# Performance work log

Measured on AMD Instinct MI355X. Metric: run time of the kernel, lower is better.

## Reference

```python
import jax, jax.numpy as jnp
import numpy as np

L = 3          # num_modification_layers
MOD_SCALE = 0.01


def setup_inputs() -> dict:
    key = jax.random.key(0)
    B, E = 8192, 1024
    ks = jax.random.split(key, 12)
    sg = 1.0 / np.sqrt(E)        # GRUCell / Linear(E,.) init bound
    sh = 1.0 / np.sqrt(E // 2)   # Linear(E//2, E) init bound
    u = lambda k, shape, s: jax.random.uniform(k, shape, jnp.float32, -s, s)
    return {
        "x":    jax.random.normal(ks[0], (B, E), jnp.float32),
        # GRUCell params (PyTorch layout: gates ordered r, z, n)
        "W_ih": u(ks[1], (L, 3 * E, E), sg),
        "W_hh": u(ks[2], (L, 3 * E, E), sg),
        "b_ih": u(ks[3], (L, 3 * E), sg),
        "b_hh": u(ks[4], (L, 3 * E), sg),
        # modification network: Linear(E, E//2) -> ReLU -> Linear(E//2, E) -> Tanh
        "W1":   u(ks[5], (L, E // 2, E), sg),
        "b1":   u(ks[6], (L, E // 2), sg),
        "W2":   u(ks[7], (L, E, E // 2), sh),
        "b2":   u(ks[8], (L, E), sh),
        # modification gate: Linear(E, 1) -> Sigmoid
        "Wg":   u(ks[9], (L, 1, E), sg),
        "bg":   u(ks[10], (L, 1), sg),
    }


def reference(x, W_ih, W_hh, b_ih, b_hh, W1, b1, W2, b2, Wg, bg):
    B, E = x.shape
    h_prev = jnp.zeros((B, E), x.dtype)  # hidden states reset to zeros
    cur = x
    for l in range(L):
        # modification network (small MLP) + scalar gate
        sig = jnp.tanh(jax.nn.relu(cur @ W1[l].T + b1[l]) @ W2[l].T + b2[l])  # (B, E)
        gate = jax.nn.sigmoid(cur @ Wg[l].T + bg[l])                           # (B, 1)
        cond = jnp.mean(gate) > 0.5
        # data-dependent self-modification: weight_ih += scale * mean(sig)[None,:]
        # (row-broadcast over the 3E gate rows), predicated on-device
        wih = jnp.where(cond,
                        W_ih[l] + MOD_SCALE * jnp.mean(sig, axis=0)[None, :],
                        W_ih[l])
        # GRUCell (PyTorch semantics)
        gi = cur @ wih.T + b_ih[l]            # (B, 3E)
        gh = h_prev @ W_hh[l].T + b_hh[l]     # (B, 3E) -- h_prev is zeros
        i_r, i_z, i_n = jnp.split(gi, 3, axis=1)
        h_r, h_z, h_n = jnp.split(gh, 3, axis=1)
        r = jax.nn.sigmoid(i_r + h_r)
        z = jax.nn.sigmoid(i_z + h_z)
        n = jnp.tanh(i_n + r * h_n)
        h = (1.0 - z) * n + z * h_prev
        cur = h + sig
    return cur
```

## Files before the change

kernel.cpp:

```cpp
#include <hip/hip_runtime.h>
#include <cstdint>
#include <cstddef>


#define BSZ 8192
#define ESZ 1024

typedef _Float16 f16x8 __attribute__((ext_vector_type(8)));
typedef float    f32x4 __attribute__((ext_vector_type(4)));
typedef unsigned short u16;
typedef u16 u16x4 __attribute__((ext_vector_type(4)));

__device__ __forceinline__ u16 f2h(float f) {
    _Float16 h = (_Float16)f;
    return __builtin_bit_cast(u16, h);
}
__device__ __forceinline__ float h2f(u16 h) {
    return (float)__builtin_bit_cast(_Float16, h);
}

__device__ __forceinline__ void gload16(const void* g, void* l) {
    __builtin_amdgcn_global_load_lds((const __attribute__((address_space(1))) void*)g,
                                     (__attribute__((address_space(3))) void*)l,
                                     16, 0, 0);
}

__device__ __forceinline__ int swzi(int row, int chunk) {
    return (row << 6) + (((chunk ^ row) & 7) << 3);
}

__device__ __forceinline__ float sigmoidf_(float x) {
    return 1.f / (1.f + __expf(-x));
}
__device__ __forceinline__ float tanhf_(float x) {
    float cx = fminf(fmaxf(x, -15.f), 15.f);
    float e = __expf(2.f * cx);
    return (e - 1.f) / (e + 1.f);
}

#define N4_WIH (3 * 3072 * 1024 / 4)
#define N4_W1  (3 * 512 * 1024 / 4)
#define N4_W2  (3 * 1024 * 512 / 4)
#define N4_X   (BSZ * ESZ / 4)

__global__ void cvt_all_kernel(const float* __restrict__ Wih, const float* __restrict__ W1,
                               const float* __restrict__ W2, const float* __restrict__ x,
                               u16* __restrict__ oWih, u16* __restrict__ oW1,
                               u16* __restrict__ oW2, u16* __restrict__ ox) {
    int i = blockIdx.x * 256 + threadIdx.x;
    const float* in;
    u16* out;
    if (i < N4_WIH) { in = Wih; out = oWih; }
    else if (i < N4_WIH + N4_W1) { i -= N4_WIH; in = W1; out = oW1; }
    else if (i < N4_WIH + N4_W1 + N4_W2) { i -= N4_WIH + N4_W1; in = W2; out = oW2; }
    else { i -= N4_WIH + N4_W1 + N4_W2; if (i >= N4_X) return; in = x; out = ox; }
    f32x4 v = ((const f32x4*)in)[i];
    u16x4 o;
    o.x = f2h(v.x); o.y = f2h(v.y); o.z = f2h(v.z); o.w = f2h(v.w);
    ((u16x4*)out)[i] = o;
}

__global__ void gate_kernel(const u16* __restrict__ cur, const float* __restrict__ Wg,
                            const float* __restrict__ bg, const float* __restrict__ colsum,
                            float* __restrict__ gsum, float* __restrict__ sdot) {
    const int wid = threadIdx.x >> 6, lane = threadIdx.x & 63;
    const int row = blockIdx.x * 4 + wid;
    const u16* cr = cur + (size_t)row * ESZ;
    float pg = 0.f, pm = 0.f;
#pragma unroll
    for (int h = 0; h < 2; h++) {
        int base = lane * 16 + h * 8;
        f16x8 cv = *(const f16x8*)(cr + base);
#pragma unroll
        for (int q = 0; q < 2; q++) {
            f32x4 wv = *(const f32x4*)(Wg + base + q * 4);
            f32x4 mv = *(const f32x4*)(colsum + base + q * 4);
#pragma unroll
            for (int e = 0; e < 4; e++) {
                float c = (float)cv[q * 4 + e];
                pg += c * wv[e];
                pm += c * mv[e];
            }
        }
    }
#pragma unroll
    for (int s = 32; s >= 1; s >>= 1) {
        pg += __shfl_xor(pg, s);
        pm += __shfl_xor(pm, s);
    }
    __shared__ float gp[4];
    if (lane == 0) {
        gp[wid] = sigmoidf_(pg + bg[0]);
        sdot[row] = pm * (0.01f / 8192.f);
    }
    __syncthreads();
    if (threadIdx.x == 0) atomicAdd(gsum, gp[0] + gp[1] + gp[2] + gp[3]);
}

template <int ACT>
__global__ void __launch_bounds__(256, 2) gemm_act_kernel(
    const u16* __restrict__ A, const u16* __restrict__ W,
    const float* __restrict__ bias, u16* __restrict__ outp,
    float* __restrict__ colsum, int N, int K) {
    __shared__ u16 lA[128 * 64];
    __shared__ u16 lB[128 * 64];
    const int t = threadIdx.x;
    const int m0 = blockIdx.y * 128, n0 = blockIdx.x * 128;
    const int wid = t >> 6, lane = t & 63;
    const int waver = wid >> 1, wavec = wid & 1;
    const int lrow = lane & 15, lk = lane >> 4;

    f32x4 acc[4][4] = {};

    for (int k0 = 0; k0 < K; k0 += 64) {
        __syncthreads();
#pragma unroll
        for (int i = 0; i < 4; i++) {
            int eo = i * 2048 + t * 8;
            int r = eo >> 6;
            int gc = (((eo >> 3) ^ r) & 7) << 3;
            gload16(A + (size_t)(m0 + r) * K + k0 + gc, &lA[eo]);
            gload16(W + (size_t)(n0 + r) * K + k0 + gc, &lB[eo]);
        }
        __syncthreads();
#pragma unroll
        for (int kk = 0; kk < 2; kk++) {
            f16x8 af[4], bf[4];
#pragma unroll
            for (int m = 0; m < 4; m++)
                af[m] = *(const f16x8*)&lA[swzi(waver * 64 + m * 16 + lrow, kk * 4 + lk)];
#pragma unroll
            for (int n = 0; n < 4; n++)
                bf[n] = *(const f16x8*)&lB[swzi(wavec * 64 + n * 16 + lrow, kk * 4 + lk)];
#pragma unroll
            for (int m = 0; m < 4; m++)
#pragma unroll
                for (int n = 0; n < 4; n++)
                    acc[m][n] = __builtin_amdgcn_mfma_f32_16x16x32_f16(af[m], bf[n], acc[m][n], 0, 0, 0);
        }
    }

#pragma unroll
    for (int n = 0; n < 4; n++) {
        int c = n0 + wavec * 64 + n * 16 + lrow;
        float bv = bias[c];
        float cs = 0.f;
#pragma unroll
        for (int m = 0; m < 4; m++) {
            int rbase = m0 + waver * 64 + m * 16 + lk * 4;
#pragma unroll
            for (int j = 0; j < 4; j++) {
                float v = acc[m][n][j] + bv;
                if (ACT == 0) {
                    v = v > 0.f ? v : 0.f;
                    outp[(size_t)(rbase + j) * N + c] = f2h(v);
                } else {
                    float tv = tanhf_(v);
                    outp[(size_t)(rbase + j) * N + c] = f2h(tv);
                    cs += tv;
                }
            }
        }
        if (ACT == 1) {
            cs += __shfl_xor(cs, 16);
            cs += __shfl_xor(cs, 32);
            if (lane < 16) atomicAdd(&colsum[c], cs);
        }
    }
}

__global__ void __launch_bounds__(256, 2) gemm_gru_kernel(
    const u16* __restrict__ Ab, const u16* __restrict__ Wb,
    const float* __restrict__ bih, const float* __restrict__ bhh,
    const u16* __restrict__ sig, const float* __restrict__ sdot,
    const float* __restrict__ gsum, float* __restrict__ curf_out,
    u16* __restrict__ curb_out) {
    __shared__ u16 lA[2][128 * 64];
    __shared__ u16 lB[2][3][64 * 64];
    const int t = threadIdx.x;
    const int hw = blockIdx.y * 16 + blockIdx.x;
    const int xcd = hw & 7, idx = hw >> 3;
    const int m0 = (idx >> 1) * 128, c0 = ((xcd << 1) | (idx & 1)) * 64;
    const int wid = t >> 6, lane = t & 63;
    const int waver = wid >> 1, wavec = wid & 1;
    const int lrow = lane & 15, lk = lane >> 4;
    const int K = ESZ, E = ESZ;

    const int eoA = t * 8;
    f32x4 acc[4][6] = {};

    auto STAGE = [&](int buf, int k0) {
#pragma unroll
        for (int i = 0; i < 4; i++) {
            int eo = i * 2048 + eoA;
            int r = eo >> 6;
            int gc = (((eo >> 3) ^ r) & 7) << 3;
            gload16(Ab + (size_t)(m0 + r) * K + k0 + gc, &lA[buf][eo]);
        }
#pragma unroll
        for (int g = 0; g < 3; g++)
#pragma unroll
            for (int i = 0; i < 2; i++) {
                int eo = i * 2048 + eoA;
                int r = eo >> 6;
                int gc = (((eo >> 3) ^ r) & 7) << 3;
                gload16(Wb + (size_t)(g * 1024 + c0 + r) * K + k0 + gc, &lB[buf][g][eo]);
            }
    };

    STAGE(0, 0);
    int cur = 0;
    for (int kt = 0; kt < 16; ++kt) {
        __syncthreads();
        if (kt < 15) STAGE(cur ^ 1, (kt + 1) * 64);
#pragma unroll
        for (int kk = 0; kk < 2; kk++) {
            f16x8 af[4];
#pragma unroll
            for (int m = 0; m < 4; m++)
                af[m] = *(const f16x8*)&lA[cur][swzi(waver * 64 + m * 16 + lrow, kk * 4 + lk)];
#pragma unroll
            for (int g = 0; g < 3; g++) {
#pragma unroll
                for (int n = 0; n < 2; n++) {
                    f16x8 bf = *(const f16x8*)&lB[cur][g][swzi(wavec * 32 + n * 16 + lrow, kk * 4 + lk)];
#pragma unroll
                    for (int m = 0; m < 4; m++)
                        acc[m][g * 2 + n] =
                            __builtin_amdgcn_mfma_f32_16x16x32_f16(af[m], bf, acc[m][g * 2 + n], 0, 0, 0);
                }
            }
        }
        cur ^= 1;
    }

    const bool cond = (*gsum) > 4096.f;
#pragma unroll
    for (int m = 0; m < 4; m++) {
        int rbase = m0 + waver * 64 + m * 16 + lk * 4;
        float corr[4];
#pragma unroll
        for (int j = 0; j < 4; j++) corr[j] = cond ? sdot[rbase + j] : 0.f;
#pragma unroll
        for (int n = 0; n < 2; n++) {
            int c = c0 + wavec * 32 + n * 16 + lrow;
            float br = bih[c], bz = bih[E + c], bn = bih[2 * E + c];
            float hr = bhh[c], hz = bhh[E + c], hn = bhh[2 * E + c];
#pragma unroll
            for (int j = 0; j < 4; j++) {
                float ir = acc[m][0 + n][j] + br + corr[j];
                float iz = acc[m][2 + n][j] + bz + corr[j];
                float inn = acc[m][4 + n][j] + bn + corr[j];
                float r = sigmoidf_(ir + hr);
                float z = sigmoidf_(iz + hz);
                float nn = tanhf_(inn + r * hn);
                float h = (1.f - z) * nn;
                float o = h + h2f(sig[(size_t)(rbase + j) * E + c]);
                if (curf_out) curf_out[(size_t)(rbase + j) * E + c] = o;
                if (curb_out) curb_out[(size_t)(rbase + j) * E + c] = f2h(o);
            }
        }
    }
}

extern "C" void kernel_launch(void* const* d_in, const int* in_sizes, int n_in,
                              void* d_out, int out_size, void* d_ws, size_t ws_size,
                              hipStream_t stream) {
    const float* x   = (const float*)d_in[0];
    const float* Wih = (const float*)d_in[1];
    const float* bih = (const float*)d_in[3];
    const float* bhh = (const float*)d_in[4];
    const float* W1  = (const float*)d_in[5];
    const float* b1  = (const float*)d_in[6];
    const float* W2  = (const float*)d_in[7];
    const float* b2  = (const float*)d_in[8];
    const float* Wg  = (const float*)d_in[9];
    const float* bg  = (const float*)d_in[10];
    float* out = (float*)d_out;

    char* w = (char*)d_ws;
    u16* Wihb  = (u16*)w;  w += (size_t)3 * 3072 * 1024 * 2;
    u16* W1b   = (u16*)w;  w += (size_t)3 * 512 * 1024 * 2;
    u16* W2b   = (u16*)w;  w += (size_t)3 * 1024 * 512 * 2;
    u16* curbA = (u16*)w;  w += (size_t)BSZ * ESZ * 2;
    u16* curbB = (u16*)w;  w += (size_t)BSZ * ESZ * 2;
    u16* Amat  = (u16*)w;  w += (size_t)BSZ * 512 * 2;
    u16* sigb  = (u16*)w;  w += (size_t)BSZ * ESZ * 2;
    float* colsum = (float*)w;  w += 4096;
    float* gsum   = (float*)w;  w += 256;
    float* sdot   = (float*)w;  w += (size_t)BSZ * 4;

    {
        int n4 = N4_WIH + N4_W1 + N4_W2 + N4_X;
        cvt_all_kernel<<<dim3((n4 + 255) / 256), 256, 0, stream>>>(
            Wih, W1, W2, x, Wihb, W1b, W2b, curbA);
    }

    u16* cin = curbA;
    u16* cout = curbB;
    for (int l = 0; l < 3; l++) {
        hipMemsetAsync(colsum, 0, 4096 + 4, stream);
        gemm_act_kernel<0><<<dim3(512 / 128, BSZ / 128), 256, 0, stream>>>(
            cin, W1b + (size_t)l * 512 * 1024, b1 + l * 512, Amat, nullptr, 512, 1024);
        gemm_act_kernel<1><<<dim3(1024 / 128, BSZ / 128), 256, 0, stream>>>(
            Amat, W2b + (size_t)l * 1024 * 512, b2 + l * 1024, sigb, colsum, 1024, 512);
        gate_kernel<<<dim3(BSZ / 4), 256, 0, stream>>>(
            cin, Wg + l * 1024, bg + l, colsum, gsum, sdot);
        gemm_gru_kernel<<<dim3(16, BSZ / 128), 256, 0, stream>>>(
            cin, Wihb + (size_t)l * 3072 * 1024, bih + l * 3072, bhh + l * 3072,
            sigb, sdot, gsum, (l == 2) ? out : nullptr, (l < 2) ? cout : nullptr);
        u16* tmp = cin; cin = cout; cout = tmp;
    }
}
```

Before: 595.5 us.

## Use 128x64 tiles, double-buffered LDS, and XCD-aware block remap in MLP GEMMs

The two modification-MLP GEMM kernels move from 128x128 to 128x64 output tiles, which doubles the grid size (256→512 and 512→1024 blocks) and raises the occupancy hint to 3 blocks per CU. Global-to-LDS loads are now double-buffered so the next K-slice is fetched while the current one feeds the MFMAs. Block IDs are remapped across the 8 XCDs so that neighbouring tiles land on the same XCD, which should improve L2 reuse. The cost is less reuse of A per tile, more total A traffic, and a larger LDS footprint per block.

After: 582.3 us. 2.2% less time.

```diff
diff --git a/kernel.cpp b/kernel.cpp
--- a/kernel.cpp
+++ b/kernel.cpp
@@ -98,51 +98,68 @@
 }
 
 template <int ACT>
-__global__ void __launch_bounds__(256, 2) gemm_act_kernel(
+__global__ void __launch_bounds__(256, 3) gemm_act_kernel(
     const u16* __restrict__ A, const u16* __restrict__ W,
     const float* __restrict__ bias, u16* __restrict__ outp,
-    float* __restrict__ colsum, int N, int K) {
-    __shared__ u16 lA[128 * 64];
-    __shared__ u16 lB[128 * 64];
+    float* __restrict__ colsum, int N, int K, int nshift) {
+    __shared__ u16 lA[2][128 * 64];
+    __shared__ u16 lB[2][64 * 64];
     const int t = threadIdx.x;
-    const int m0 = blockIdx.y * 128, n0 = blockIdx.x * 128;
+    const int chunk = gridDim.x >> 3;
+    const int o = blockIdx.x;
+    const int tl = (o & 7) * chunk + (o >> 3);
+    const int m0 = (tl >> nshift) * 128;
+    const int n0 = (tl & ((1 << nshift) - 1)) * 64;
     const int wid = t >> 6, lane = t & 63;
     const int waver = wid >> 1, wavec = wid & 1;
     const int lrow = lane & 15, lk = lane >> 4;
 
-    f32x4 acc[4][4] = {};
-
-    for (int k0 = 0; k0 < K; k0 += 64) {
-        __syncthreads();
+    f32x4 acc[4][2] = {};
+
+    auto STAGE = [&](int buf, int k0) {
 #pragma unroll
         for (int i = 0; i < 4; i++) {
             int eo = i * 2048 + t * 8;
             int r = eo >> 6;
             int gc = (((eo >> 3) ^ r) & 7) << 3;
-            gload16(A + (size_t)(m0 + r) * K + k0 + gc, &lA[eo]);
-            gload16(W + (size_t)(n0 + r) * K + k0 + gc, &lB[eo]);
-        }
+            gload16(A + (size_t)(m0 + r) * K + k0 + gc, &lA[buf][eo]);
+        }
+#pragma unroll
+        for (int i = 0; i < 2; i++) {
+            int eo = i * 2048 + t * 8;
+            int r = eo >> 6;
+            int gc = (((eo >> 3) ^ r) & 7) << 3;
+            gload16(W + (size_t)(n0 + r) * K + k0 + gc, &lB[buf][eo]);
+        }
+    };
+
+    STAGE(0, 0);
+    const int nk = K >> 6;
+    int cur = 0;
+    for (int kt = 0; kt < nk; ++kt) {
         __syncthreads();
+        if (kt + 1 < nk) STAGE(cur ^ 1, (kt + 1) * 64);
 #pragma unroll
         for (int kk = 0; kk < 2; kk++) {
-            f16x8 af[4], bf[4];
+            f16x8 af[4], bf[2];
 #pragma unroll
             for (int m = 0; m < 4; m++)
-                af[m] = *(const f16x8*)&lA[swzi(waver * 64 + m * 16 + lrow, kk * 4 + lk)];
-#pragma unroll
-            for (int n = 0; n < 4; n++)
-                bf[n] = *(const f16x8*)&lB[swzi(wavec * 64 + n * 16 + lrow, kk * 4 + lk)];
+                af[m] = *(const f16x8*)&lA[cur][swzi(waver * 64 + m * 16 + lrow, kk * 4 + lk)];
+#pragma unroll
+            for (int n = 0; n < 2; n++)
+                bf[n] = *(const f16x8*)&lB[cur][swzi(wavec * 32 + n * 16 + lrow, kk * 4 + lk)];
 #pragma unroll
             for (int m = 0; m < 4; m++)
 #pragma unroll
-                for (int n = 0; n < 4; n++)
+                for (int n = 0; n < 2; n++)
                     acc[m][n] = __builtin_amdgcn_mfma_f32_16x16x32_f16(af[m], bf[n], acc[m][n], 0, 0, 0);
         }
-    }
-
-#pragma unroll
-    for (int n = 0; n < 4; n++) {
-        int c = n0 + wavec * 64 + n * 16 + lrow;
+        cur ^= 1;
+    }
+
+#pragma unroll
+    for (int n = 0; n < 2; n++) {
+        int c = n0 + wavec * 32 + n * 16 + lrow;
         float bv = bias[c];
         float cs = 0.f;
 #pragma unroll
@@ -300,10 +317,10 @@
     u16* cout = curbB;
     for (int l = 0; l < 3; l++) {
         hipMemsetAsync(colsum, 0, 4096 + 4, stream);
-        gemm_act_kernel<0><<<dim3(512 / 128, BSZ / 128), 256, 0, stream>>>(
-            cin, W1b + (size_t)l * 512 * 1024, b1 + l * 512, Amat, nullptr, 512, 1024);
-        gemm_act_kernel<1><<<dim3(1024 / 128, BSZ / 128), 256, 0, stream>>>(
-            Amat, W2b + (size_t)l * 1024 * 512, b2 + l * 1024, sigb, colsum, 1024, 512);
+        gemm_act_kernel<0><<<dim3(512), 256, 0, stream>>>(
+            cin, W1b + (size_t)l * 512 * 1024, b1 + l * 512, Amat, nullptr, 512, 1024, 3);
+        gemm_act_kernel<1><<<dim3(1024), 256, 0, stream>>>(
+            Amat, W2b + (size_t)l * 1024 * 512, b2 + l * 1024, sigb, colsum, 1024, 512, 4);
         gate_kernel<<<dim3(BSZ / 4), 256, 0, stream>>>(
             cin, Wg + l * 1024, bg + l, colsum, gsum, sdot);
         gemm_gru_kernel<<<dim3(16, BSZ / 128), 256, 0, stream>>>(
```

## Unify GEMMs into one 512-thread double-buffered kernel with 256-row tiles

Applied to the files above, without the earlier changes.

Replaces the separate activation GEMM and GRU GEMM kernels with a single templated kernel. It uses 512 threads (8 waves), 256-row A tiles, double-buffered LDS staging and XCD-aware block mapping. The MLP GEMMs now get the prefetch pipelining the GRU GEMM already had, and larger M tiles reuse each staged B tile across more rows. The cost is more LDS per block (the GRU variant needs about 128KB with double buffering), which can lower occupancy. Narrower 64-column N tiles for the MLP GEMMs mean the A tile is reloaded more often.

After: 581.0 us. -2.4%, faster.

```diff
diff --git a/kernel.cpp b/kernel.cpp
--- a/kernel.cpp
+++ b/kernel.cpp
@@ -97,122 +97,50 @@
     if (threadIdx.x == 0) atomicAdd(gsum, gp[0] + gp[1] + gp[2] + gp[3]);
 }
 
-template <int ACT>
-__global__ void __launch_bounds__(256, 2) gemm_act_kernel(
+template <int NG, int EPI>
+__global__ void __launch_bounds__(512, 2) gemm_fused_kernel(
     const u16* __restrict__ A, const u16* __restrict__ W,
-    const float* __restrict__ bias, u16* __restrict__ outp,
-    float* __restrict__ colsum, int N, int K) {
-    __shared__ u16 lA[128 * 64];
-    __shared__ u16 lB[128 * 64];
+    const float* __restrict__ bias, const float* __restrict__ bhh,
+    const u16* __restrict__ sig, const float* __restrict__ sdot,
+    const float* __restrict__ gsum, u16* __restrict__ outp,
+    float* __restrict__ curf_out, float* __restrict__ colsum,
+    int K, int NC) {
+    __shared__ u16 lA[2][256 * 64];
+    __shared__ u16 lB[2][NG][64 * 64];
     const int t = threadIdx.x;
-    const int m0 = blockIdx.y * 128, n0 = blockIdx.x * 128;
+    const int xcd = blockIdx.x & 7, q = blockIdx.x >> 3;
+    const int m0 = (xcd * 4 + (q & 3)) * 256;
+    const int c0 = (q >> 2) * 64;
     const int wid = t >> 6, lane = t & 63;
     const int waver = wid >> 1, wavec = wid & 1;
     const int lrow = lane & 15, lk = lane >> 4;
-
-    f32x4 acc[4][4] = {};
-
-    for (int k0 = 0; k0 < K; k0 += 64) {
-        __syncthreads();
+    const int E = ESZ;
+
+    f32x4 acc[4][2 * NG] = {};
+
+    auto STAGE = [&](int buf, int k0) {
 #pragma unroll
         for (int i = 0; i < 4; i++) {
-            int eo = i * 2048 + t * 8;
+            int eo = i * 4096 + t * 8;
             int r = eo >> 6;
             int gc = (((eo >> 3) ^ r) & 7) << 3;
-            gload16(A + (size_t)(m0 + r) * K + k0 + gc, &lA[eo]);
-            gload16(W + (size_t)(n0 + r) * K + k0 + gc, &lB[eo]);
-        }
-        __syncthreads();
-#pragma unroll
-        for (int kk = 0; kk < 2; kk++) {
-            f16x8 af[4], bf[4];
-#pragma unroll
-            for (int m = 0; m < 4; m++)
-                af[m] = *(const f16x8*)&lA[swzi(waver * 64 + m * 16 + lrow, kk * 4 + lk)];
-#pragma unroll
-            for (int n = 0; n < 4; n++)
-                bf[n] = *(const f16x8*)&lB[swzi(wavec * 64 + n * 16 + lrow, kk * 4 + lk)];
-#pragma unroll
-            for (int m = 0; m < 4; m++)
-#pragma unroll
-                for (int n = 0; n < 4; n++)
-                    acc[m][n] = __builtin_amdgcn_mfma_f32_16x16x32_f16(af[m], bf[n], acc[m][n], 0, 0, 0);
-        }
-    }
-
-#pragma unroll
-    for (int n = 0; n < 4; n++) {
-        int c = n0 + wavec * 64 + n * 16 + lrow;
-        float bv = bias[c];
-        float cs = 0.f;
-#pragma unroll
-        for (int m = 0; m < 4; m++) {
-            int rbase = m0 + waver * 64 + m * 16 + lk * 4;
-#pragma unroll
-            for (int j = 0; j < 4; j++) {
-                float v = acc[m][n][j] + bv;
-                if (ACT == 0) {
-                    v = v > 0.f ? v : 0.f;
-                    outp[(size_t)(rbase + j) * N + c] = f2h(v);
-                } else {
-                    float tv = tanhf_(v);
-                    outp[(size_t)(rbase + j) * N + c] = f2h(tv);
-                    cs += tv;
-                }
-            }
-        }
-        if (ACT == 1) {
-            cs += __shfl_xor(cs, 16);
-            cs += __shfl_xor(cs, 32);
-            if (lane < 16) atomicAdd(&colsum[c], cs);
-        }
-    }
-}
-
-__global__ void __launch_bounds__(256, 2) gemm_gru_kernel(
-    const u16* __restrict__ Ab, const u16* __restrict__ Wb,
-    const float* __restrict__ bih, const float* __restrict__ bhh,
-    const u16* __restrict__ sig, const float* __restrict__ sdot,
-    const float* __restrict__ gsum, float* __restrict__ curf_out,
-    u16* __restrict__ curb_out) {
-    __shared__ u16 lA[2][128 * 64];
-    __shared__ u16 lB[2][3][64 * 64];
-    const int t = threadIdx.x;
-    const int hw = blockIdx.y * 16 + blockIdx.x;
-    const int xcd = hw & 7, idx = hw >> 3;
-    const int m0 = (idx >> 1) * 128, c0 = ((xcd << 1) | (idx & 1)) * 64;
-    const int wid = t >> 6, lane = t & 63;
-    const int waver = wid >> 1, wavec = wid & 1;
-    const int lrow = lane & 15, lk = lane >> 4;
-    const int K = ESZ, E = ESZ;
-
-    const int eoA = t * 8;
-    f32x4 acc[4][6] = {};
-
-    auto STAGE = [&](int buf, int k0) {
-#pragma unroll
-        for (int i = 0; i < 4; i++) {
-            int eo = i * 2048 + eoA;
+            gload16(A + (size_t)(m0 + r) * K + k0 + gc, &lA[buf][eo]);
+        }
+#pragma unroll
+        for (int g = 0; g < NG; g++) {
+            int eo = t * 8;
             int r = eo >> 6;
             int gc = (((eo >> 3) ^ r) & 7) << 3;
-            gload16(Ab + (size_t)(m0 + r) * K + k0 + gc, &lA[buf][eo]);
-        }
-#pragma unroll
-        for (int g = 0; g < 3; g++)
-#pragma unroll
-            for (int i = 0; i < 2; i++) {
-                int eo = i * 2048 + eoA;
-                int r = eo >> 6;
-                int gc = (((eo >> 3) ^ r) & 7) << 3;
-                gload16(Wb + (size_t)(g * 1024 + c0 + r) * K + k0 + gc, &lB[buf][g][eo]);
-            }
+            gload16(W + (size_t)(g * 1024 + c0 + r) * K + k0 + gc, &lB[buf][g][eo]);
+        }
     };
 
     STAGE(0, 0);
+    const int nk = K >> 6;
     int cur = 0;
-    for (int kt = 0; kt < 16; ++kt) {
+    for (int kt = 0; kt < nk; ++kt) {
         __syncthreads();
-        if (kt < 15) STAGE(cur ^ 1, (kt + 1) * 64);
+        if (kt + 1 < nk) STAGE(cur ^ 1, (kt + 1) * 64);
 #pragma unroll
         for (int kk = 0; kk < 2; kk++) {
             f16x8 af[4];
@@ -220,7 +148,7 @@
             for (int m = 0; m < 4; m++)
                 af[m] = *(const f16x8*)&lA[cur][swzi(waver * 64 + m * 16 + lrow, kk * 4 + lk)];
 #pragma unroll
-            for (int g = 0; g < 3; g++) {
+            for (int g = 0; g < NG; g++) {
 #pragma unroll
                 for (int n = 0; n < 2; n++) {
                     f16x8 bf = *(const f16x8*)&lB[cur][g][swzi(wavec * 32 + n * 16 + lrow, kk * 4 + lk)];
@@ -234,30 +162,61 @@
         cur ^= 1;
     }
 
-    const bool cond = (*gsum) > 4096.f;
-#pragma unroll
-    for (int m = 0; m < 4; m++) {
-        int rbase = m0 + waver * 64 + m * 16 + lk * 4;
-        float corr[4];
-#pragma unroll
-        for (int j = 0; j < 4; j++) corr[j] = cond ? sdot[rbase + j] : 0.f;
+    if (EPI == 2) {
+        const bool cond = (*gsum) > 4096.f;
+#pragma unroll
+        for (int m = 0; m < 4; m++) {
+            int rbase = m0 + waver * 64 + m * 16 + lk * 4;
+            float corr[4];
+#pragma unroll
+            for (int j = 0; j < 4; j++) corr[j] = cond ? sdot[rbase + j] : 0.f;
+#pragma unroll
+            for (int n = 0; n < 2; n++) {
+                int c = c0 + wavec * 32 + n * 16 + lrow;
+                float br = bias[c], bz = bias[E + c], bn = bias[2 * E + c];
+                float hr = bhh[c], hz = bhh[E + c], hn = bhh[2 * E + c];
+#pragma unroll
+                for (int j = 0; j < 4; j++) {
+                    float ir = acc[m][0 + n][j] + br + corr[j];
+                    float iz = acc[m][2 + n][j] + bz + corr[j];
+                    float inn = acc[m][4 + n][j] + bn + corr[j];
+                    float r = sigmoidf_(ir + hr);
+                    float z = sigmoidf_(iz + hz);
+                    float nn = tanhf_(inn + r * hn);
+                    float h = (1.f - z) * nn;
+                    float o = h + h2f(sig[(size_t)(rbase + j) * E + c]);
+                    if (curf_out) curf_out[(size_t)(rbase + j) * E + c] = o;
+                    if (outp) outp[(size_t)(rbase + j) * E + c] = f2h(o);
+                }
+            }
+        }
+    } else {
+        const int N = NC << 6;
 #pragma unroll
         for (int n = 0; n < 2; n++) {
             int c = c0 + wavec * 32 + n * 16 + lrow;
-            float br = bih[c], bz = bih[E + c], bn = bih[2 * E + c];
-            float hr = bhh[c], hz = bhh[E + c], hn = bhh[2 * E + c];
-#pragma unroll
-            for (int j = 0; j < 4; j++) {
-                float ir = acc[m][0 + n][j] + br + corr[j];
-                float iz = acc[m][2 + n][j] + bz + corr[j];
-                float inn = acc[m][4 + n][j] + bn + corr[j];
-                float r = sigmoidf_(ir + hr);
-                float z = sigmoidf_(iz + hz);
-                float nn = tanhf_(inn + r * hn);
-                float h = (1.f - z) * nn;
-                float o = h + h2f(sig[(size_t)(rbase + j) * E + c]);
-                if (curf_out) curf_out[(size_t)(rbase + j) * E + c] = o;
-                if (curb_out) curb_out[(size_t)(rbase + j) * E + c] = f2h(o);
+            float bv = bias[c];
+            float cs = 0.f;
+#pragma unroll
+            for (int m = 0; m < 4; m++) {
+                int rbase = m0 + waver * 64 + m * 16 + lk * 4;
+#pragma unroll
+                for (int j = 0; j < 4; j++) {
+                    float v = acc[m][n][j] + bv;
+                    if (EPI == 0) {
+                        v = v > 0.f ? v : 0.f;
+                        outp[(size_t)(rbase + j) * N + c] = f2h(v);
+                    } else {
+                        float tv = tanhf_(v);
+                        outp[(size_t)(rbase + j) * N + c] = f2h(tv);
+                        cs += tv;
+                    }
+                }
+            }
+            if (EPI == 1) {
+                cs += __shfl_xor(cs, 16);
+                cs += __shfl_xor(cs, 32);
+                if (lane < 16) atomicAdd(&colsum[c], cs);
             }
         }
     }
@@ -300,15 +259,18 @@
     u16* cout = curbB;
     for (int l = 0; l < 3; l++) {
         hipMemsetAsync(colsum, 0, 4096 + 4, stream);
-        gemm_act_kernel<0><<<dim3(512 / 128, BSZ / 128), 256, 0, stream>>>(
-            cin, W1b + (size_t)l * 512 * 1024, b1 + l * 512, Amat, nullptr, 512, 1024);
-        gemm_act_kernel<1><<<dim3(1024 / 128, BSZ / 128), 256, 0, stream>>>(
-            Amat, W2b + (size_t)l * 1024 * 512, b2 + l * 1024, sigb, colsum, 1024, 512);
+        gemm_fused_kernel<1, 0><<<dim3(32 * 8), 512, 0, stream>>>(
+            cin, W1b + (size_t)l * 512 * 1024, b1 + l * 512, nullptr,
+            nullptr, nullptr, nullptr, Amat, nullptr, nullptr, 1024, 8);
+        gemm_fused_kernel<1, 1><<<dim3(32 * 16), 512, 0, stream>>>(
+            Amat, W2b + (size_t)l * 1024 * 512, b2 + l * 1024, nullptr,
+            nullptr, nullptr, nullptr, sigb, nullptr, colsum, 512, 16);
         gate_kernel<<<dim3(BSZ / 4), 256, 0, stream>>>(
             cin, Wg + l * 1024, bg + l, colsum, gsum, sdot);
-        gemm_gru_kernel<<<dim3(16, BSZ / 128), 256, 0, stream>>>(
+        gemm_fused_kernel<3, 2><<<dim3(32 * 16), 512, 0, stream>>>(
             cin, Wihb + (size_t)l * 3072 * 1024, bih + l * 3072, bhh + l * 3072,
-            sigb, sdot, gsum, (l == 2) ? out : nullptr, (l < 2) ? cout : nullptr);
+            sigb, sdot, gsum, (l < 2) ? cout : nullptr,
+            (l == 2) ? out : nullptr, nullptr, 1024, 16);
         u16* tmp = cin; cin = cout; cout = tmp;
     }
 }
```
